# Optimization experiments

Measured on AMD Instinct MI355X. Metric: run time of the kernel, lower is better.

The kernel has to match this reference:

```python
import jax, jax.numpy as jnp
import numpy as np
from math import log

X_SIZE, Y_SIZE, W_SIZE = 512, 512, 256
SIGMA = 2.0
TIME_CONST = 1000.0 / log(SIGMA)  # default time_constant = 1000/log(sigma)


def setup_inputs() -> dict:
    key = jax.random.key(0)
    k1, k2 = jax.random.split(key)
    x = jax.random.normal(k1, (W_SIZE,), dtype=jnp.float32)
    W = jax.random.normal(k2, (X_SIZE, Y_SIZE, W_SIZE), dtype=jnp.float32)
    return {"x": x, "W": W, "time_step": 100}


def reference(x, W, time_step):
    # per-cell L2 distance: (X_SIZE, Y_SIZE)
    d = jnp.linalg.norm(x - W, ord=2, axis=-1)
    flat = jnp.argmin(d)
    wx, wy = jnp.unravel_index(flat, (X_SIZE, Y_SIZE))
    # torch.meshgrid default 'ij' indexing
    GX, GY = jnp.meshgrid(
        jnp.arange(X_SIZE, dtype=jnp.float32),
        jnp.arange(Y_SIZE, dtype=jnp.float32),
        indexing="ij",
    )
    decay = SIGMA * jnp.exp(-jnp.float32(time_step) / TIME_CONST)
    denom = 2.0 * decay * decay
    # Faithful to torch: GX.T[wx, wy] == wy and GY.T[wx, wy] == wx
    distx = (GX - wy.astype(jnp.float32)) ** 2
    disty = (GY - wx.astype(jnp.float32)) ** 2
    h = (jnp.exp(-distx / denom) * jnp.exp(-disty / denom)).T
    return h, (wx, wy)
```

## Files before the change

### kernel.cpp

```cpp
#include <hip/hip_runtime.h>
#include <math.h>

#define XS 512
#define YS 512
#define WDIM 256
#define NCELLS (XS * YS)
#define K1_BLOCKS 2048
#define K1_THREADS 256

__global__ __launch_bounds__(K1_THREADS) void som_dist_kernel(
    const float* __restrict__ x,
    const float* __restrict__ W,
    unsigned long long* __restrict__ ws) {
  const int lane = threadIdx.x & 63;
  const int waveInBlock = threadIdx.x >> 6;
  const int gw = blockIdx.x * (K1_THREADS / 64) + waveInBlock;

  const float4 xv = ((const float4*)x)[lane];

  float bestD = 3.4e38f;
  int bestI = 0;

  const int base = gw * 32;
#pragma unroll 4
  for (int c = 0; c < 32; ++c) {
    const int cell = base + c;
    const float4 wv = *((const float4*)(W + (size_t)cell * WDIM) + lane);
    const float dx = xv.x - wv.x;
    const float dy = xv.y - wv.y;
    const float dz = xv.z - wv.z;
    const float dw = xv.w - wv.w;
    float s = dx * dx + dy * dy + dz * dz + dw * dw;
#pragma unroll
    for (int off = 32; off > 0; off >>= 1) s += __shfl_xor(s, off, 64);
    if (s < bestD) { bestD = s; bestI = cell; }
  }

  const unsigned long long packed =
      ((unsigned long long)__float_as_uint(bestD) << 32) | (unsigned int)bestI;

  __shared__ unsigned long long sbest[K1_THREADS / 64];
  if (lane == 0) sbest[waveInBlock] = packed;
  __syncthreads();
  if (threadIdx.x == 0) {
    unsigned long long m = sbest[0];
#pragma unroll
    for (int i = 1; i < K1_THREADS / 64; ++i) {
      const unsigned long long v = sbest[i];
      m = (v < m) ? v : m;
    }
    ws[blockIdx.x] = m;
  }
}

__global__ __launch_bounds__(256) void som_h_kernel(
    const unsigned long long* __restrict__ ws,
    const int* __restrict__ time_step,
    float* __restrict__ out) {
  __shared__ unsigned long long red[256];
  const int t = threadIdx.x;

  unsigned long long m = 0xFFFFFFFFFFFFFFFFULL;
#pragma unroll
  for (int k = 0; k < K1_BLOCKS / 256; ++k) {
    const unsigned long long v = ws[t + 256 * k];
    m = (v < m) ? v : m;
  }
  red[t] = m;
  __syncthreads();
  for (int s = 128; s > 0; s >>= 1) {
    if (t < s) {
      const unsigned long long v = red[t + s];
      if (v < red[t]) red[t] = v;
    }
    __syncthreads();
  }
  const int flat = (int)(red[0] & 0xFFFFFFFFULL);
  const int wx = flat >> 9;
  const int wy = flat & (YS - 1);

  const float ts = (float)(*time_step);
  const float TIME_CONST = 1442.6950408889634f;
  const float decay = 2.0f * expf(-ts / TIME_CONST);
  const float denom = 2.0f * decay * decay;
  const float inv = -1.0f / denom;

  const int e = blockIdx.x * 1024 + t * 4;
  const int i = e >> 9;
  const int j0 = e & (YS - 1);
  const float di = (float)(i - wx);
  const float di2 = di * di;

  float4 r;
  {
    const float d0 = (float)(j0 + 0 - wy);
    const float d1 = (float)(j0 + 1 - wy);
    const float d2 = (float)(j0 + 2 - wy);
    const float d3 = (float)(j0 + 3 - wy);
    r.x = expf((di2 + d0 * d0) * inv);
    r.y = expf((di2 + d1 * d1) * inv);
    r.z = expf((di2 + d2 * d2) * inv);
    r.w = expf((di2 + d3 * d3) * inv);
  }
  ((float4*)out)[e >> 2] = r;

  if (blockIdx.x == 0 && t == 0) {
    out[NCELLS] = (float)wx;
    out[NCELLS + 1] = (float)wy;
  }
}

extern "C" void kernel_launch(void* const* d_in, const int* in_sizes, int n_in,
                              void* d_out, int out_size, void* d_ws, size_t ws_size,
                              hipStream_t stream) {
  const float* x = (const float*)d_in[0];
  const float* W = (const float*)d_in[1];
  const int* ts = (const int*)d_in[2];
  float* out = (float*)d_out;
  unsigned long long* ws = (unsigned long long*)d_ws;

  som_dist_kernel<<<K1_BLOCKS, K1_THREADS, 0, stream>>>(x, W, ws);
  som_h_kernel<<<NCELLS / 1024, 256, 0, stream>>>(ws, ts, out);
}
```

Baseline: 364.4 us.

## Reduce argmin via global atomicMin and use nontemporal loads for W

Each distance block now folds its best packed (distance, index) value into one global word with atomicMin, initialised by a memset. This removes the per-block workspace array and the full 2048-entry reduction that every h-kernel block used to redo. W is read with nontemporal loads and the inner loop unroll goes from 4 to 8 to push more memory traffic through the streaming pass. The cost is an extra memset launch and contended 64-bit atomics.

Result: faster. 346.8 us (-4.8%).

```diff
diff --git a/kernel.cpp b/kernel.cpp
--- a/kernel.cpp
+++ b/kernel.cpp
@@ -8,6 +8,8 @@
 #define K1_BLOCKS 2048
 #define K1_THREADS 256
 
+typedef float vfloat4 __attribute__((ext_vector_type(4)));
+
 __global__ __launch_bounds__(K1_THREADS) void som_dist_kernel(
     const float* __restrict__ x,
     const float* __restrict__ W,
@@ -16,16 +18,17 @@
   const int waveInBlock = threadIdx.x >> 6;
   const int gw = blockIdx.x * (K1_THREADS / 64) + waveInBlock;
 
-  const float4 xv = ((const float4*)x)[lane];
+  const vfloat4 xv = ((const vfloat4*)x)[lane];
 
   float bestD = 3.4e38f;
   int bestI = 0;
 
   const int base = gw * 32;
-#pragma unroll 4
+#pragma unroll 8
   for (int c = 0; c < 32; ++c) {
     const int cell = base + c;
-    const float4 wv = *((const float4*)(W + (size_t)cell * WDIM) + lane);
+    const vfloat4* p = (const vfloat4*)(W + (size_t)cell * WDIM) + lane;
+    const vfloat4 wv = __builtin_nontemporal_load(p);
     const float dx = xv.x - wv.x;
     const float dy = xv.y - wv.y;
     const float dz = xv.z - wv.z;
@@ -49,7 +52,7 @@
       const unsigned long long v = sbest[i];
       m = (v < m) ? v : m;
     }
-    ws[blockIdx.x] = m;
+    atomicMin(ws, m);
   }
 }
 
@@ -57,25 +60,9 @@
     const unsigned long long* __restrict__ ws,
     const int* __restrict__ time_step,
     float* __restrict__ out) {
-  __shared__ unsigned long long red[256];
   const int t = threadIdx.x;
-
-  unsigned long long m = 0xFFFFFFFFFFFFFFFFULL;
-#pragma unroll
-  for (int k = 0; k < K1_BLOCKS / 256; ++k) {
-    const unsigned long long v = ws[t + 256 * k];
-    m = (v < m) ? v : m;
-  }
-  red[t] = m;
-  __syncthreads();
-  for (int s = 128; s > 0; s >>= 1) {
-    if (t < s) {
-      const unsigned long long v = red[t + s];
-      if (v < red[t]) red[t] = v;
-    }
-    __syncthreads();
-  }
-  const int flat = (int)(red[0] & 0xFFFFFFFFULL);
+  const unsigned long long packed = *ws;
+  const int flat = (int)(packed & 0xFFFFFFFFULL);
   const int wx = flat >> 9;
   const int wy = flat & (YS - 1);
 
@@ -91,18 +78,16 @@
   const float di = (float)(i - wx);
   const float di2 = di * di;
 
-  float4 r;
-  {
-    const float d0 = (float)(j0 + 0 - wy);
-    const float d1 = (float)(j0 + 1 - wy);
-    const float d2 = (float)(j0 + 2 - wy);
-    const float d3 = (float)(j0 + 3 - wy);
-    r.x = expf((di2 + d0 * d0) * inv);
-    r.y = expf((di2 + d1 * d1) * inv);
-    r.z = expf((di2 + d2 * d2) * inv);
-    r.w = expf((di2 + d3 * d3) * inv);
-  }
-  ((float4*)out)[e >> 2] = r;
+  const float d0 = (float)(j0 + 0 - wy);
+  const float d1 = (float)(j0 + 1 - wy);
+  const float d2 = (float)(j0 + 2 - wy);
+  const float d3 = (float)(j0 + 3 - wy);
+  vfloat4 r;
+  r.x = expf((di2 + d0 * d0) * inv);
+  r.y = expf((di2 + d1 * d1) * inv);
+  r.z = expf((di2 + d2 * d2) * inv);
+  r.w = expf((di2 + d3 * d3) * inv);
+  ((vfloat4*)out)[e >> 2] = r;
 
   if (blockIdx.x == 0 && t == 0) {
     out[NCELLS] = (float)wx;
@@ -119,6 +104,7 @@
   float* out = (float*)d_out;
   unsigned long long* ws = (unsigned long long*)d_ws;
 
+  (void)hipMemsetAsync(ws, 0xFF, 8, stream);
   som_dist_kernel<<<K1_BLOCKS, K1_THREADS, 0, stream>>>(x, W, ws);
   som_h_kernel<<<NCELLS / 1024, 256, 0, stream>>>(ws, ts, out);
 }
```
